# Kernel tuning notes

Measured on AMD Instinct MI355X. Metric: run time of the kernel, lower is better.

## Reference

```python
import jax, jax.numpy as jnp
import numpy as np

K = 4  # recurrent_kernel_size


def setup_inputs() -> dict:
    key = jax.random.key(0)
    k1, k2, k3, k4 = jax.random.split(key, 4)
    b, t, d = 4, 4096, 1024
    x = jax.random.normal(k1, (b, t, d), dtype=jnp.float32)
    W_conv = jax.random.normal(k2, (d, 1, K), dtype=jnp.float32) * (1.0 / np.sqrt(K))
    W_proj = jax.random.normal(k3, (4 * d, d), dtype=jnp.float32) * (1.0 / np.sqrt(d))
    W_out = jax.random.normal(k4, (d, d), dtype=jnp.float32) * (1.0 / np.sqrt(d))
    return {"x": x, "W_conv": W_conv, "W_proj": W_proj, "W_out": W_out}


def _causal_dwconv(x_btd, W_conv):
    # x: [b,t,d]; W_conv: [d,1,k] (torch depthwise layout). Causal: left-pad k-1.
    d = x_btd.shape[-1]
    x_bdt = jnp.transpose(x_btd, (0, 2, 1))  # [b,d,t]
    y = jax.lax.conv_general_dilated(
        x_bdt, W_conv,
        window_strides=(1,),
        padding=[(K - 1, 0)],
        feature_group_count=d,
        dimension_numbers=("NCH", "OIH", "NCH"),
    )
    return jnp.transpose(y, (0, 2, 1))  # [b,t,d]


def reference(x, W_conv, W_proj, W_out):
    b, t, d = x.shape
    mixed = _causal_dwconv(x, W_conv)
    u = jnp.einsum("btd,ed->bte", x + mixed, W_proj)  # [b,t,4d]
    v, gate, decay, inject = jnp.split(u, 4, axis=-1)
    gate = jax.nn.sigmoid(gate)
    decay = jax.nn.sigmoid(decay)
    inject = jnp.tanh(inject)

    def step(state, inp):
        dec_t, inj_t, g_t, v_t = inp  # each [b,d]
        state = dec_t * state + (1.0 - dec_t) * inj_t
        out = g_t * v_t + (1.0 - g_t) * state
        return state, out

    # move time to leading axis for scan: [t,b,d]
    seq = (jnp.swapaxes(decay, 0, 1), jnp.swapaxes(inject, 0, 1),
           jnp.swapaxes(gate, 0, 1), jnp.swapaxes(v, 0, 1))
    state0 = jnp.zeros((b, d), dtype=x.dtype)
    _, y_tbd = jax.lax.scan(step, state0, seq)
    y = jnp.swapaxes(y_tbd, 0, 1)  # [b,t,d]
    return jnp.einsum("btd,ed->bte", y, W_out)
```

## Files before the change

### kernel.cpp

```cpp
#include <hip/hip_runtime.h>
#include <hip/hip_bf16.h>
#include <math.h>

typedef __hip_bfloat16 bf16;
typedef __bf16 bf16x8 __attribute__((ext_vector_type(8)));
typedef float f32x4 __attribute__((ext_vector_type(4)));

#define BB 4
#define TT 4096
#define DD 1024

__device__ __forceinline__ float fast_sigmoid(float x) {
  return 1.0f / (1.0f + __expf(-x));
}
__device__ __forceinline__ float fast_tanh(float x) {
  return 2.0f / (1.0f + __expf(-2.0f * x)) - 1.0f;
}

__global__ __launch_bounds__(256) void w2bf_kernel(const float* __restrict__ w,
                                                   bf16* __restrict__ o,
                                                   int n) {
  int i = blockIdx.x * 256 + threadIdx.x;
  if (i < n) o[i] = __float2bfloat16(w[i]);
}

__global__ __launch_bounds__(256) void conv_add_kernel(
    const float* __restrict__ x, const float* __restrict__ Wc,
    bf16* __restrict__ xm, int total) {
  int i = blockIdx.x * 256 + threadIdx.x;
  if (i >= total) return;
  int c = i % DD;
  int t = (i / DD) % TT;
  float w0 = Wc[c * 4 + 0], w1 = Wc[c * 4 + 1], w2 = Wc[c * 4 + 2],
        w3 = Wc[c * 4 + 3];
  float xv = x[i];
  float acc = xv + w3 * xv;
  if (t >= 1) acc += w2 * x[i - DD];
  if (t >= 2) acc += w1 * x[i - 2 * DD];
  if (t >= 3) acc += w0 * x[i - 3 * DD];
  xm[i] = __float2bfloat16(acc);
}

template <int EP>
__global__ __launch_bounds__(512) void gemm256_kernel(
    const bf16* __restrict__ A, const bf16* __restrict__ B,
    void* __restrict__ C, int M, int N, int K, int MB) {
  __shared__ __align__(16) bf16 As[2][2][128][64];
  __shared__ __align__(16) bf16 Bs[2][2][128][64];

  const int tid = threadIdx.x;
  const int wv = tid >> 6, l = tid & 63;
  const int wm = wv >> 2, wn = wv & 3;

  const int nwg = gridDim.x;
  const int cpx = nwg >> 3;
  const int bid = blockIdx.x;
  const int wg = (bid & 7) * cpx + (bid >> 3);
  const int bm = wg % MB, bn = wg / MB;
  const int m0 = bm * 256, n0 = bn * 256;

  const int lr3 = l >> 3;
  const int gcolE = ((l & 7) * 8) ^ ((l >= 32) ? 16 : 0);
  const int l15 = l & 15;
  const int xorE = (l & 4) ? 16 : 0;
  const int lhi8 = (l >> 4) * 8;
  const int colK[2] = {lhi8 ^ xorE, (32 + lhi8) ^ xorE};

  const bf16* Arow = A + (size_t)(m0 + wv * 16 + lr3) * K + gcolE;
  const bf16* Brow = B + (size_t)(n0 + wv * 16 + lr3) * K + gcolE;

  auto stage = [&](int ht) {
    const int kt = ht >> 2, which = ht & 3;
    const int slot = kt & 1;
    const int k0 = kt * 64;
    if (which < 2) {
      const int half = which;
#pragma unroll
      for (int j = 0; j < 2; ++j) {
        const bf16* src = Brow + (size_t)(half * 128 + j * 8) * K + k0;
        __builtin_amdgcn_global_load_lds(
            (const __attribute__((address_space(1))) void*)src,
            (__attribute__((address_space(3))) void*)(&Bs[slot][half][0][0] +
                                                      wv * 1024 + j * 512),
            16, 0, 0);
      }
    } else {
      const int half = which - 2;
#pragma unroll
      for (int j = 0; j < 2; ++j) {
        const bf16* src = Arow + (size_t)(half * 128 + j * 8) * K + k0;
        __builtin_amdgcn_global_load_lds(
            (const __attribute__((address_space(1))) void*)src,
            (__attribute__((address_space(3))) void*)(&As[slot][half][0][0] +
                                                      wv * 1024 + j * 512),
            16, 0, 0);
      }
    }
  };

  f32x4 acc[8][4];
#pragma unroll
  for (int i = 0; i < 8; ++i)
#pragma unroll
    for (int j = 0; j < 4; ++j) acc[i][j] = (f32x4)0.0f;

  const int NT2 = K >> 7;
  const int nht = (K >> 6) * 4;

#pragma unroll
  for (int h = 0; h < 6; ++h) stage(h);
  asm volatile("s_waitcnt vmcnt(4)" ::: "memory");
  __builtin_amdgcn_s_barrier();

  bf16x8 aF[4][2], bF0[2][2], bF1[2][2];

#pragma unroll 1
  for (int t = 0; t < NT2; ++t) {
#pragma unroll
    for (int g = 0; g < 8; ++g) {
      const int q = g & 3, grp = g >> 2;
      const bf16* ar = &As[grp][wm][0][0];
      const bf16* br = &Bs[grp][wn >> 1][0][0] + (wn & 1) * 4096;
      if (q == 0) {
#pragma unroll
        for (int mi = 0; mi < 4; ++mi)
#pragma unroll
          for (int ks = 0; ks < 2; ++ks)
            aF[mi][ks] =
                *(const bf16x8*)(ar + (mi * 16 + l15) * 64 + colK[ks]);
#pragma unroll
        for (int ni = 0; ni < 2; ++ni)
#pragma unroll
          for (int ks = 0; ks < 2; ++ks)
            bF0[ni][ks] =
                *(const bf16x8*)(br + (ni * 16 + l15) * 64 + colK[ks]);
      } else if (q == 1) {
#pragma unroll
        for (int ni = 0; ni < 2; ++ni)
#pragma unroll
          for (int ks = 0; ks < 2; ++ks)
            bF1[ni][ks] =
                *(const bf16x8*)(br + ((ni + 2) * 16 + l15) * 64 + colK[ks]);
      } else if (q == 2) {
#pragma unroll
        for (int mi = 0; mi < 4; ++mi)
#pragma unroll
          for (int ks = 0; ks < 2; ++ks)
            aF[mi][ks] =
                *(const bf16x8*)(ar + ((mi + 4) * 16 + l15) * 64 + colK[ks]);
      }
      {
        const int ht = 8 * t + 6 + g;
        if (ht < nht) stage(ht);
      }
      __builtin_amdgcn_sched_barrier(0);
      __builtin_amdgcn_s_barrier();
      __builtin_amdgcn_s_setprio(1);
#pragma unroll
      for (int mi = 0; mi < 4; ++mi)
#pragma unroll
        for (int nj = 0; nj < 2; ++nj)
#pragma unroll
          for (int ks = 0; ks < 2; ++ks)
            acc[mi + (q >= 2 ? 4 : 0)][nj + ((q & 1) ? 2 : 0)] =
                __builtin_amdgcn_mfma_f32_16x16x32_bf16(
                    aF[mi][ks], (q & 1) ? bF1[nj][ks] : bF0[nj][ks],
                    acc[mi + (q >= 2 ? 4 : 0)][nj + ((q & 1) ? 2 : 0)], 0, 0,
                    0);
      __builtin_amdgcn_s_setprio(0);
      if (g == 3) {
        if (t == NT2 - 1)
          asm volatile("s_waitcnt vmcnt(0)" ::: "memory");
        else
          asm volatile("s_waitcnt vmcnt(4)" ::: "memory");
      } else if (g == 7) {
        asm volatile("s_waitcnt vmcnt(4)" ::: "memory");
      }
      __builtin_amdgcn_sched_barrier(0);
      __builtin_amdgcn_s_barrier();
    }
  }

#pragma unroll
  for (int mi = 0; mi < 8; ++mi) {
    const int row = m0 + wm * 128 + mi * 16 + (l >> 4) * 4;
#pragma unroll
    for (int ni = 0; ni < 4; ++ni) {
      const int col = n0 + wn * 64 + ni * 16 + l15;
#pragma unroll
      for (int j = 0; j < 4; ++j) {
        float v = acc[mi][ni][j];
        if (EP == 0) {
          ((float*)C)[(size_t)(row + j) * N + col] = v;
        } else {
          const int cls = col >> 10;
          if (cls == 1 || cls == 2) v = fast_sigmoid(v);
          else if (cls == 3) v = fast_tanh(v);
          ((bf16*)C)[(size_t)(row + j) * N + col] = __float2bfloat16(v);
        }
      }
    }
  }
}

#define BM 64
#define BN 64
#define BKK 16
__global__ __launch_bounds__(256) void gemm_nt_kernel(
    const bf16* __restrict__ A, const float* __restrict__ B,
    float* __restrict__ C, int M, int N, int K) {
  __shared__ float Asm[BKK][BM + 1];
  __shared__ float Bsm[BKK][BN + 1];
  const int n0 = blockIdx.x * BN;
  const int m0 = blockIdx.y * BM;
  const int tid = threadIdx.x;
  const int tx = tid & 15, ty = tid >> 4;
  const int lk = tid & 15, lr = tid >> 4;
  float acc[4][4] = {};
  for (int k0 = 0; k0 < K; k0 += BKK) {
#pragma unroll
    for (int p = 0; p < 4; ++p) {
      Asm[lk][lr + 16 * p] =
          __bfloat162float(A[(size_t)(m0 + lr + 16 * p) * K + (k0 + lk)]);
      Bsm[lk][lr + 16 * p] = B[(size_t)(n0 + lr + 16 * p) * K + (k0 + lk)];
    }
    __syncthreads();
#pragma unroll
    for (int kk = 0; kk < BKK; ++kk) {
      float a[4], b[4];
#pragma unroll
      for (int i = 0; i < 4; ++i) a[i] = Asm[kk][ty * 4 + i];
#pragma unroll
      for (int j = 0; j < 4; ++j) b[j] = Bsm[kk][tx * 4 + j];
#pragma unroll
      for (int i = 0; i < 4; ++i)
#pragma unroll
        for (int j = 0; j < 4; ++j) acc[i][j] += a[i] * b[j];
    }
    __syncthreads();
  }
#pragma unroll
  for (int i = 0; i < 4; ++i)
#pragma unroll
    for (int j = 0; j < 4; ++j)
      C[(size_t)(m0 + ty * 4 + i) * N + (n0 + tx * 4 + j)] = acc[i][j];
}

__global__ __launch_bounds__(256) void scan_chunk_kernel(
    const bf16* __restrict__ u, float* __restrict__ cA,
    float* __restrict__ cB, int nchunk, int tchunk) {
  int idx = blockIdx.x * 256 + threadIdx.x;
  int c = idx % DD;
  int chunk = (idx / DD) % nchunk;
  int b = idx / (DD * nchunk);
  const bf16* ub = u + (size_t)b * TT * 4 * DD;
  float Aacc = 1.0f, Bacc = 0.0f;
  int t0 = chunk * tchunk;
  for (int t = t0; t < t0 + tchunk; ++t) {
    const bf16* row = ub + (size_t)t * 4 * DD;
    float dec = __bfloat162float(row[2 * DD + c]);
    float inj = __bfloat162float(row[3 * DD + c]);
    Aacc *= dec;
    Bacc = dec * Bacc + (1.0f - dec) * inj;
  }
  cA[idx] = Aacc;
  cB[idx] = Bacc;
}

__global__ __launch_bounds__(256) void scan_prefix_kernel(
    const float* __restrict__ cA, const float* __restrict__ cB,
    float* __restrict__ S, int nchunk) {
  int idx = blockIdx.x * 256 + threadIdx.x;
  int c = idx % DD;
  int b = idx / DD;
  float s = 0.0f;
  for (int j = 0; j < nchunk; ++j) {
    int e = (b * nchunk + j) * DD + c;
    S[e] = s;
    s = cA[e] * s + cB[e];
  }
}

__global__ __launch_bounds__(256) void scan_out_kernel(
    const bf16* __restrict__ u, const float* __restrict__ S,
    bf16* __restrict__ y, int nchunk, int tchunk) {
  int idx = blockIdx.x * 256 + threadIdx.x;
  int c = idx % DD;
  int chunk = (idx / DD) % nchunk;
  int b = idx / (DD * nchunk);
  const bf16* ub = u + (size_t)b * TT * 4 * DD;
  bf16* yb = y + (size_t)b * TT * DD;
  float state = S[idx];
  int t0 = chunk * tchunk;
  for (int t = t0; t < t0 + tchunk; ++t) {
    const bf16* row = ub + (size_t)t * 4 * DD;
    float v = __bfloat162float(row[c]);
    float g = __bfloat162float(row[DD + c]);
    float dec = __bfloat162float(row[2 * DD + c]);
    float inj = __bfloat162float(row[3 * DD + c]);
    state = dec * state + (1.0f - dec) * inj;
    yb[(size_t)t * DD + c] = __float2bfloat16(g * v + (1.0f - g) * state);
  }
}

extern "C" void kernel_launch(void* const* d_in, const int* in_sizes, int n_in,
                              void* d_out, int out_size, void* d_ws,
                              size_t ws_size, hipStream_t stream) {
  const float* x = (const float*)d_in[0];
  const float* Wc = (const float*)d_in[1];
  const float* Wp = (const float*)d_in[2];
  const float* Wo = (const float*)d_in[3];
  float* out = (float*)d_out;

  const size_t nb = (size_t)TT * DD;

  auto need = [&](int nbat, int nchunk, bool wob) -> size_t {
    return (size_t)nbat * nb * 2 + (size_t)nbat * 4 * nb * 2 +
           (size_t)4 * DD * DD * 2 + (wob ? (size_t)DD * DD * 2 : 0) +
           (size_t)3 * nbat * nchunk * DD * 4;
  };

  int nbat, nchunk;
  bool haveWob;
  if (ws_size >= need(4, 64, true)) {
    nbat = 4; nchunk = 64; haveWob = true;
  } else if (ws_size >= need(1, 64, true)) {
    nbat = 1; nchunk = 64; haveWob = true;
  } else {
    nbat = 1; nchunk = 16; haveWob = false;
  }
  const int tchunk = TT / nchunk;

  char* p = (char*)d_ws;
  bf16* Wpb = (bf16*)p;  p += (size_t)4 * DD * DD * 2;
  bf16* Wob = nullptr;
  if (haveWob) { Wob = (bf16*)p; p += (size_t)DD * DD * 2; }
  bf16* xm = (bf16*)p;   p += (size_t)nbat * nb * 2;
  bf16* u = (bf16*)p;    p += (size_t)nbat * 4 * nb * 2;
  float* cA = (float*)p; p += (size_t)nbat * nchunk * DD * 4;
  float* cB = (float*)p; p += (size_t)nbat * nchunk * DD * 4;
  float* S = (float*)p;
  bf16* y = xm;

  w2bf_kernel<<<(4 * DD * DD) / 256, 256, 0, stream>>>(Wp, Wpb, 4 * DD * DD);
  if (haveWob)
    w2bf_kernel<<<(DD * DD) / 256, 256, 0, stream>>>(Wo, Wob, DD * DD);

  for (int b0 = 0; b0 < BB; b0 += nbat) {
    const float* xb = x + (size_t)b0 * nb;
    float* outb = out + (size_t)b0 * nb;
    const int Mtot = nbat * TT;
    const int total = (int)(nbat * nb);

    conv_add_kernel<<<total / 256, 256, 0, stream>>>(xb, Wc, xm, total);

    {
      const int MB = Mtot / 256;
      const int nwg = MB * (4 * DD / 256);
      gemm256_kernel<1><<<nwg, 512, 0, stream>>>(xm, Wpb, u, Mtot, 4 * DD, DD,
                                                 MB);
    }
    {
      int nthreads = nbat * nchunk * DD;
      scan_chunk_kernel<<<nthreads / 256, 256, 0, stream>>>(u, cA, cB, nchunk,
                                                            tchunk);
      scan_prefix_kernel<<<(nbat * DD) / 256, 256, 0, stream>>>(cA, cB, S,
                                                                nchunk);
      scan_out_kernel<<<nthreads / 256, 256, 0, stream>>>(u, S, y, nchunk,
                                                          tchunk);
    }
    if (haveWob) {
      const int MB = Mtot / 256;
      const int nwg = MB * (DD / 256);
      gemm256_kernel<0><<<nwg, 512, 0, stream>>>(y, Wob, outb, Mtot, DD, DD,
                                                 MB);
    } else {
      dim3 grid(DD / BN, Mtot / BM);
      gemm_nt_kernel<<<grid, 256, 0, stream>>>(y, Wo, outb, Mtot, DD, DD);
    }
  }
}
```

Before: 372.4 us.

## Vectorize conv and scan kernels, remap GEMM tile swizzle and LDS XOR pattern

The conv kernel now handles four channels per thread with 128-bit float loads. The scan chunk and scan output kernels handle eight channels per thread with 128-bit bf16 loads and stores, which cuts instruction count and raises bytes per memory transaction. The GEMM changes its workgroup-to-tile mapping so each XCD gets a contiguous band of M tiles, and changes the LDS XOR swizzle to a full row-based XOR to reduce bank conflicts. Having 8x fewer threads in the scan kernels may lower occupancy and latency hiding for the sequential loops, and the new swizzle must match the rest of the unseen load code to stay correct.

```diff
diff --git a/kernel.cpp b/kernel.cpp
--- a/kernel.cpp
+++ b/kernel.cpp
@@ -5,6 +5,9 @@
 typedef __hip_bfloat16 bf16;
 typedef __bf16 bf16x8 __attribute__((ext_vector_type(8)));
 typedef float f32x4 __attribute__((ext_vector_type(4)));
+typedef float f32x4v __attribute__((ext_vector_type(4)));
+typedef unsigned short u16x8v __attribute__((ext_vector_type(8)));
+typedef unsigned short u16x4v __attribute__((ext_vector_type(4)));
 
 #define BB 4
 #define TT 4096
@@ -15,6 +18,16 @@
 }
 __device__ __forceinline__ float fast_tanh(float x) {
   return 2.0f / (1.0f + __expf(-2.0f * x)) - 1.0f;
+}
+__device__ __forceinline__ float b2f(unsigned short u) {
+  union { unsigned int i; float f; } x;
+  x.i = ((unsigned int)u) << 16;
+  return x.f;
+}
+__device__ __forceinline__ unsigned short f2b(float f) {
+  union { bf16 h; unsigned short u; } x;
+  x.h = __float2bfloat16(f);
+  return x.u;
 }
 
 __global__ __launch_bounds__(256) void w2bf_kernel(const float* __restrict__ w,
@@ -26,19 +39,25 @@
 
 __global__ __launch_bounds__(256) void conv_add_kernel(
     const float* __restrict__ x, const float* __restrict__ Wc,
-    bf16* __restrict__ xm, int total) {
+    bf16* __restrict__ xm, int total4) {
   int i = blockIdx.x * 256 + threadIdx.x;
-  if (i >= total) return;
-  int c = i % DD;
-  int t = (i / DD) % TT;
-  float w0 = Wc[c * 4 + 0], w1 = Wc[c * 4 + 1], w2 = Wc[c * 4 + 2],
-        w3 = Wc[c * 4 + 3];
-  float xv = x[i];
-  float acc = xv + w3 * xv;
-  if (t >= 1) acc += w2 * x[i - DD];
-  if (t >= 2) acc += w1 * x[i - 2 * DD];
-  if (t >= 3) acc += w0 * x[i - 3 * DD];
-  xm[i] = __float2bfloat16(acc);
+  if (i >= total4) return;
+  int c4 = (i & (DD / 4 - 1)) * 4;
+  int t = (i / (DD / 4)) % TT;
+  size_t base = (size_t)i * 4;
+  f32x4v x0 = *(const f32x4v*)(x + base);
+  f32x4v p1 = (t >= 1) ? *(const f32x4v*)(x + base - DD) : (f32x4v)0.0f;
+  f32x4v p2 = (t >= 2) ? *(const f32x4v*)(x + base - 2 * DD) : (f32x4v)0.0f;
+  f32x4v p3 = (t >= 3) ? *(const f32x4v*)(x + base - 3 * DD) : (f32x4v)0.0f;
+  u16x4v o;
+#pragma unroll
+  for (int j = 0; j < 4; ++j) {
+    f32x4v w = *(const f32x4v*)(Wc + (size_t)(c4 + j) * 4);
+    float acc = x0[j] + w[3] * x0[j] + w[2] * p1[j] + w[1] * p2[j] +
+                w[0] * p3[j];
+    o[j] = f2b(acc);
+  }
+  *(u16x4v*)(xm + base) = o;
 }
 
 template <int EP>
@@ -52,19 +71,19 @@
   const int wv = tid >> 6, l = tid & 63;
   const int wm = wv >> 2, wn = wv & 3;
 
-  const int nwg = gridDim.x;
-  const int cpx = nwg >> 3;
   const int bid = blockIdx.x;
-  const int wg = (bid & 7) * cpx + (bid >> 3);
-  const int bm = wg % MB, bn = wg / MB;
+  const int xcd = bid & 7, ii = bid >> 3;
+  const int mb8 = MB >> 3;
+  const int bm = xcd * mb8 + (ii % mb8);
+  const int bn = ii / mb8;
   const int m0 = bm * 256, n0 = bn * 256;
 
   const int lr3 = l >> 3;
-  const int gcolE = ((l & 7) * 8) ^ ((l >= 32) ? 16 : 0);
+  const int gcolE = ((l & 7) ^ (l >> 3)) * 8;
   const int l15 = l & 15;
-  const int xorE = (l & 4) ? 16 : 0;
+  const int rxor = (l15 & 7) << 3;
   const int lhi8 = (l >> 4) * 8;
-  const int colK[2] = {lhi8 ^ xorE, (32 + lhi8) ^ xorE};
+  const int colK[2] = {lhi8 ^ rxor, (32 + lhi8) ^ rxor};
 
   const bf16* Arow = A + (size_t)(m0 + wv * 16 + lr3) * K + gcolE;
   const bf16* Brow = B + (size_t)(n0 + wv * 16 + lr3) * K + gcolE;
@@ -250,21 +269,28 @@
     const bf16* __restrict__ u, float* __restrict__ cA,
     float* __restrict__ cB, int nchunk, int tchunk) {
   int idx = blockIdx.x * 256 + threadIdx.x;
-  int c = idx % DD;
-  int chunk = (idx / DD) % nchunk;
-  int b = idx / (DD * nchunk);
+  int c8 = (idx & (DD / 8 - 1)) * 8;
+  int chunk = (idx / (DD / 8)) % nchunk;
+  int b = idx / ((DD / 8) * nchunk);
   const bf16* ub = u + (size_t)b * TT * 4 * DD;
-  float Aacc = 1.0f, Bacc = 0.0f;
+  float Aacc[8], Bacc[8];
+#pragma unroll
+  for (int j = 0; j < 8; ++j) { Aacc[j] = 1.0f; Bacc[j] = 0.0f; }
   int t0 = chunk * tchunk;
   for (int t = t0; t < t0 + tchunk; ++t) {
     const bf16* row = ub + (size_t)t * 4 * DD;
-    float dec = __bfloat162float(row[2 * DD + c]);
-    float inj = __bfloat162float(row[3 * DD + c]);
-    Aacc *= dec;
-    Bacc = dec * Bacc + (1.0f - dec) * inj;
-  }
-  cA[idx] = Aacc;
-  cB[idx] = Bacc;
+    u16x8v dv = *(const u16x8v*)(row + 2 * DD + c8);
+    u16x8v iv = *(const u16x8v*)(row + 3 * DD + c8);
+#pragma unroll
+    for (int j = 0; j < 8; ++j) {
+      float dec = b2f(dv[j]), inj = b2f(iv[j]);
+      Aacc[j] *= dec;
+      Bacc[j] = dec * Bacc[j] + (1.0f - dec) * inj;
+    }
+  }
+  int base = (b * nchunk + chunk) * DD + c8;
+#pragma unroll
+  for (int j = 0; j < 8; ++j) { cA[base + j] = Aacc[j]; cB[base + j] = Bacc[j]; }
 }
 
 __global__ __launch_bounds__(256) void scan_prefix_kernel(
@@ -285,21 +311,31 @@
     const bf16* __restrict__ u, const float* __restrict__ S,
     bf16* __restrict__ y, int nchunk, int tchunk) {
   int idx = blockIdx.x * 256 + threadIdx.x;
-  int c = idx % DD;
-  int chunk = (idx / DD) % nchunk;
-  int b = idx / (DD * nchunk);
+  int c8 = (idx & (DD / 8 - 1)) * 8;
+  int chunk = (idx / (DD / 8)) % nchunk;
+  int b = idx / ((DD / 8) * nchunk);
   const bf16* ub = u + (size_t)b * TT * 4 * DD;
   bf16* yb = y + (size_t)b * TT * DD;
-  float state = S[idx];
+  float st[8];
+  int sbase = (b * nchunk + chunk) * DD + c8;
+#pragma unroll
+  for (int j = 0; j < 8; ++j) st[j] = S[sbase + j];
   int t0 = chunk * tchunk;
   for (int t = t0; t < t0 + tchunk; ++t) {
     const bf16* row = ub + (size_t)t * 4 * DD;
-    float v = __bfloat162float(row[c]);
-    float g = __bfloat162float(row[DD + c]);
-    float dec = __bfloat162float(row[2 * DD + c]);
-    float inj = __bfloat162float(row[3 * DD + c]);
-    state = dec * state + (1.0f - dec) * inj;
-    yb[(size_t)t * DD + c] = __float2bfloat16(g * v + (1.0f - g) * state);
+    u16x8v vv = *(const u16x8v*)(row + c8);
+    u16x8v gv = *(const u16x8v*)(row + DD + c8);
+    u16x8v dv = *(const u16x8v*)(row + 2 * DD + c8);
+    u16x8v iv = *(const u16x8v*)(row + 3 * DD + c8);
+    u16x8v ov;
+#pragma unroll
+    for (int j = 0; j < 8; ++j) {
+      float dec = b2f(dv[j]), inj = b2f(iv[j]);
+      float g = b2f(gv[j]), v = b2f(vv[j]);
+      st[j] = dec * st[j] + (1.0f - dec) * inj;
+      ov[j] = f2b(g * v + (1.0f - g) * st[j]);
+    }
+    *(u16x8v*)(yb + (size_t)t * DD + c8) = ov;
   }
 }
 
@@ -350,9 +386,9 @@
     const float* xb = x + (size_t)b0 * nb;
     float* outb = out + (size_t)b0 * nb;
     const int Mtot = nbat * TT;
-    const int total = (int)(nbat * nb);
-
-    conv_add_kernel<<<total / 256, 256, 0, stream>>>(xb, Wc, xm, total);
+    const int total4 = (int)(nbat * nb / 4);
+
+    conv_add_kernel<<<total4 / 256, 256, 0, stream>>>(xb, Wc, xm, total4);
 
     {
       const int MB = Mtot / 256;
@@ -361,7 +397,7 @@
                                                  MB);
     }
     {
-      int nthreads = nbat * nchunk * DD;
+      int nthreads = nbat * nchunk * (DD / 8);
       scan_chunk_kernel<<<nthreads / 256, 256, 0, stream>>>(u, cA, cB, nchunk,
                                                             tchunk);
       scan_prefix_kernel<<<(nbat * DD) / 256, 256, 0, stream>>>(cA, cB, S,
```

Measured after the change: 318.0 us. 14.6% less time.
